# Kernel optimization log

Hardware: AMD Instinct MI355X
Metric: run time of the kernel (lower is better)

The kernel has to match this reference:

```python
import jax, jax.numpy as jnp
import numpy as np

P = 45007
VEC = 4            # default_vec in the triton kernel
BK = 32            # BLOCK_SIZE_K
BN = 32            # BLOCK_SIZE_N
REDN = 2           # reduction factor
IN_FEATURES = 4096
OUT_FEATURES = 4096
RED_IN = ((IN_FEATURES // REDN + BK - 1) // BK) * BK  # 2048


def build_full_idx(random_numbers, K, N, red_in, bk, bn, redn, vec):
    """Vectorized port of SSL.get_idx: flat indices into weight.flatten() for the
    expanded (K, N) weight (i.e. full_weight^T)."""
    R0 = random_numbers[0].astype(jnp.int32)
    R1 = random_numbers[1].astype(jnp.int32)
    R2 = random_numbers[2].astype(jnp.int32)
    R3 = random_numbers[3].astype(jnp.int32)
    ni = K // bk   # number of K blocks
    nj = N // bn   # number of N blocks
    i = jnp.arange(ni, dtype=jnp.int32)
    j = jnp.arange(nj, dtype=jnp.int32)
    it = i // redn                 # [ni]
    itin = i % redn                # [ni]
    h = R3 + R2 * j[None, :] + R1 * (it[:, None] + 1)   # [ni, nj]
    h1 = R0 * (itin + 1)                                 # [ni]
    offset = bk - ((h + h1[:, None]) * vec) % bk         # [ni, nj]
    locs = (offset[:, :, None] + jnp.arange(bk, dtype=jnp.int32)) % bk  # [ni, nj, bk]
    # row index into the compressed weight's reduced-K axis
    row_red = it[:, None, None] * bk + locs              # [ni, nj, bk]
    # reorder so k = i*bk + kk is the leading axis: (ni, bk, nj) -> (K, nj)
    row_red = jnp.transpose(row_red, (0, 2, 1)).reshape(K, nj)
    row_full = jnp.repeat(row_red, bn, axis=1)           # [K, N]
    n_idx = jnp.arange(N, dtype=jnp.int32)[None, :]
    return n_idx * red_in + row_full                     # flat index into weight.flatten()


def setup_inputs() -> dict:
    key = jax.random.key(0)
    k1, k2, k3 = jax.random.split(key, 3)
    x = jax.random.normal(k1, (4, 2048, IN_FEATURES), dtype=jnp.float32)
    # xavier_uniform over (out_features, red_in_features)
    bound_w = float(np.sqrt(6.0 / (OUT_FEATURES + RED_IN)))
    weight = jax.random.uniform(k2, (OUT_FEATURES, RED_IN), dtype=jnp.float32,
                                minval=-bound_w, maxval=bound_w)
    bound_b = 1.0 / float(np.sqrt(IN_FEATURES))
    bias = jax.random.uniform(k3, (OUT_FEATURES,), dtype=jnp.float32,
                              minval=-bound_b, maxval=bound_b)
    # random_numbers = cat([P], 3 ints in [0, P)); fixed representative values
    random_numbers = jnp.array([P, 12345, 6789, 23456], dtype=jnp.int32)
    return {"x": x, "weight": weight, "bias": bias, "random_numbers": random_numbers}


def reference(x, weight, bias, random_numbers):
    K = x.shape[-1]
    N = weight.shape[0]
    full_idx = build_full_idx(random_numbers, K, N, RED_IN, BK, BN, REDN, VEC)  # [K, N]
    w_full = weight.reshape(-1)[full_idx]            # [K, N] = expanded weight^T
    x2 = x.reshape(-1, K)                            # [M, K]
    y = x2 @ w_full + bias[None, :]                  # [M, N]
    return y.reshape(*x.shape[:-1], N)
```

## Files before the change

kernel.cpp:

```cpp
#include <hip/hip_runtime.h>

typedef __bf16 bf16x8 __attribute__((ext_vector_type(8)));
typedef float  f32x4  __attribute__((ext_vector_type(4)));
typedef unsigned short ushort8 __attribute__((ext_vector_type(8)));

#define KDIM  4096
#define NDIM  4096
#define REDIN 2048

static __device__ __forceinline__ unsigned short f2bf(float f) {
    return __builtin_bit_cast(unsigned short, (__bf16)f);
}

typedef __attribute__((address_space(3))) void       lds_void;
typedef const __attribute__((address_space(1))) void gbl_cvoid;

static __device__ __forceinline__ void gload16(const void* g, void* l) {
    __builtin_amdgcn_global_load_lds((gbl_cvoid*)g, (lds_void*)l, 16, 0, 0);
}

__global__ void cvt_x(const float* __restrict__ x, unsigned short* __restrict__ xb,
                      long n8) {
    long idx = (long)blockIdx.x * blockDim.x + threadIdx.x;
    long stride = (long)gridDim.x * blockDim.x;
    for (long i = idx; i < n8; i += stride) {
        const float4 a = ((const float4*)x)[2 * i];
        const float4 b = ((const float4*)x)[2 * i + 1];
        ushort8 s;
        s[0] = f2bf(a.x); s[1] = f2bf(a.y); s[2] = f2bf(a.z); s[3] = f2bf(a.w);
        s[4] = f2bf(b.x); s[5] = f2bf(b.y); s[6] = f2bf(b.z); s[7] = f2bf(b.w);
        ((ushort8*)xb)[i] = s;
    }
}

__global__ void expand_w(const float* __restrict__ w, unsigned short* __restrict__ wx,
                         const int* __restrict__ rn) {
    const int R0 = rn[0], R1 = rn[1], R2 = rn[2], R3 = rn[3];
    const long total = (long)NDIM * (KDIM / 8);
    long idx = (long)blockIdx.x * blockDim.x + threadIdx.x;
    long stride = (long)gridDim.x * blockDim.x;
    for (long t = idx; t < total; t += stride) {
        const int kp = (int)(t & (KDIM / 8 - 1));
        const int n  = (int)(t >> 9);
        const int k0 = kp * 8;
        const int i  = k0 >> 5;
        const int kk0 = k0 & 31;
        const int it = i >> 1;
        const int h  = R3 + R2 * (n >> 5) + R1 * (it + 1) + R0 * ((i & 1) + 1);
        const int off = 32 - ((h << 2) & 31);
        const float* src = w + (long)n * REDIN + it * 32;
        ushort8 s;
#pragma unroll
        for (int q = 0; q < 8; ++q)
            s[q] = f2bf(src[(kk0 + q + off) & 31]);
        ((ushort8*)wx)[t] = s;
    }
}


#define STAGE_T(T)                                                          \
  {                                                                         \
    const int _b  = (T) & 3;                                                \
    const long _ko = (long)(T) * 32;                                        \
    gload16(srcA1 + _ko, ldsA + _b * 8192 + dst1);                          \
    gload16(srcA2 + _ko, ldsA + _b * 8192 + dst2);                          \
    gload16(srcB1 + _ko, ldsB + _b * 8192 + dst1);                          \
    gload16(srcB2 + _ko, ldsB + _b * 8192 + dst2);                          \
  }

#define KBODY(T, CUR, NXT, DOSTAGE, VMSTR)                                  \
  {                                                                         \
    if (DOSTAGE) STAGE_T((T) + 3);                                          \
    asm volatile("s_waitcnt vmcnt(" VMSTR ")" ::: "memory");                \
    __builtin_amdgcn_sched_barrier(0);                                      \
    __builtin_amdgcn_s_barrier();                                           \
    __builtin_amdgcn_sched_barrier(0);                                      \
    const char* _pa = (const char*)ldsA + ((T) & 3) * 16384 + aOff;         \
    const char* _pb = (const char*)ldsB + (((T) + 1) & 3) * 16384 + bOff;   \
    _Pragma("unroll")                                                       \
    for (int _n = 0; _n < 4; ++_n)                                          \
      bf##NXT[_n] = *(const bf16x8*)(_pb + _n * 1024);                      \
    _Pragma("unroll")                                                       \
    for (int _m = 0; _m < 8; ++_m)                                          \
      af[_m] = *(const bf16x8*)(_pa + _m * 1024);                           \
    _Pragma("unroll")                                                       \
    for (int _m = 0; _m < 8; ++_m)                                          \
      _Pragma("unroll")                                                     \
      for (int _n = 0; _n < 4; ++_n)                                        \
        acc[_m][_n] = __builtin_amdgcn_mfma_f32_16x16x32_bf16(              \
            af[_m], bf##CUR[_n], acc[_m][_n], 0, 0, 0);                     \
    asm volatile("s_waitcnt lgkmcnt(0)" ::: "memory");                      \
    __builtin_amdgcn_sched_barrier(0);                                      \
    __builtin_amdgcn_s_barrier();                                           \
  }

__global__ __launch_bounds__(512, 2)
void gemm_bt256(const unsigned short* __restrict__ A,
                const unsigned short* __restrict__ B,
                const float* __restrict__ bias,
                float* __restrict__ out, int M)
{
    __shared__ __align__(16) unsigned short ldsA[4 * 8192];
    __shared__ __align__(16) unsigned short ldsB[4 * 8192];

    const int nwg = gridDim.x;
    const int bid = blockIdx.x;
    int swzb = bid;
    if ((nwg & 7) == 0) {
        const int cpx = nwg >> 3;
        swzb = (bid & 7) * cpx + (bid >> 3);
    }
    const int ntn = NDIM / 256;
    const int n0 = (swzb % ntn) * 256;
    const int m0 = (swzb / ntn) * 256;

    const int tid  = threadIdx.x;
    const int lane = tid & 63;
    const int wid  = tid >> 6;
    const int wr   = wid >> 2;
    const int wc   = wid & 3;
    const int lrow = lane & 15;

    const int sswz = (tid & 3) ^ ((tid >> 3) & 3);
    const int dst1 = tid * 8;
    const int dst2 = tid * 8 + 4096;
    const unsigned short* srcA1 = A + (size_t)(m0 + (tid >> 2)) * KDIM + 8 * sswz;
    const unsigned short* srcA2 = srcA1 + (size_t)128 * KDIM;
    const unsigned short* srcB1 = B + (size_t)(n0 + (tid >> 2)) * KDIM + 8 * sswz;
    const unsigned short* srcB2 = srcB1 + (size_t)128 * KDIM;

    const int rswz = (lane >> 4) ^ ((lane >> 1) & 3);
    const int aOff = (wr * 128 + lrow) * 64 + (rswz << 4);
    const int bOff = (wc * 64 + lrow) * 64 + (rswz << 4);

    f32x4 acc[8][4];
#pragma unroll
    for (int m = 0; m < 8; ++m)
#pragma unroll
        for (int n = 0; n < 4; ++n)
            acc[m][n] = (f32x4)(0.0f);

    bf16x8 af[8], bfA[4], bfB[4];

    STAGE_T(0);
    STAGE_T(1);
    STAGE_T(2);
    asm volatile("s_waitcnt vmcnt(8)" ::: "memory");
    __builtin_amdgcn_sched_barrier(0);
    __builtin_amdgcn_s_barrier();
    __builtin_amdgcn_sched_barrier(0);
    {
        const char* _pb = (const char*)ldsB + bOff;
#pragma unroll
        for (int n = 0; n < 4; ++n)
            bfA[n] = *(const bf16x8*)(_pb + n * 1024);
    }

    for (int tt = 0; tt < 124; tt += 2) {
        KBODY(tt,     A, B, true, "8");
        KBODY(tt + 1, B, A, true, "8");
    }
    KBODY(124, A, B, true,  "8");
    KBODY(125, B, A, false, "4");
    KBODY(126, A, B, false, "0");
    {
        const char* _pa = (const char*)ldsA + 3 * 16384 + aOff;
#pragma unroll
        for (int m = 0; m < 8; ++m)
            af[m] = *(const bf16x8*)(_pa + m * 1024);
#pragma unroll
        for (int m = 0; m < 8; ++m)
#pragma unroll
            for (int n = 0; n < 4; ++n)
                acc[m][n] = __builtin_amdgcn_mfma_f32_16x16x32_bf16(
                    af[m], bfB[n], acc[m][n], 0, 0, 0);
    }

#pragma unroll
    for (int n = 0; n < 4; ++n) {
        const int col = n0 + wc * 64 + n * 16 + lrow;
        const float bv = bias[col];
#pragma unroll
        for (int m = 0; m < 8; ++m) {
            const size_t rbase = (size_t)(m0 + wr * 128 + m * 16 + (lane >> 4) * 4);
#pragma unroll
            for (int e = 0; e < 4; ++e)
                out[(rbase + e) * NDIM + col] = acc[m][n][e] + bv;
        }
    }
}

__global__ __launch_bounds__(256, 2)
void ssl_gemm_fused(const float* __restrict__ x, const float* __restrict__ w,
                    const float* __restrict__ bias, const int* __restrict__ rn,
                    float* __restrict__ out)
{
    __shared__ __align__(16) unsigned short As[128][40];
    __shared__ __align__(16) unsigned short Bs[128][40];

    const int R0 = rn[0], R1 = rn[1], R2 = rn[2], R3 = rn[3];
    const int tid = threadIdx.x;
    const int n0 = blockIdx.x * 128;
    const int m0 = blockIdx.y * 128;
    const int srow = tid >> 3;
    const int scol = (tid & 7) * 4;
    const int lane = tid & 63;
    const int wid  = tid >> 6;
    const int wr   = wid >> 1;
    const int wc   = wid & 1;
    const int lrow = lane & 15;
    const int lk   = (lane >> 4) * 8;

    f32x4 acc[4][4];
#pragma unroll
    for (int m = 0; m < 4; ++m)
#pragma unroll
        for (int n = 0; n < 4; ++n)
            acc[m][n] = (f32x4)(0.0f);

    for (int i = 0; i < KDIM / 32; ++i) {
        const int it   = i >> 1;
        const int k0   = i * 32;
#pragma unroll
        for (int p = 0; p < 4; ++p) {
            const int row = p * 32 + srow;
            const float4 v = *(const float4*)(x + (size_t)(m0 + row) * KDIM + k0 + scol);
            ushort4 s;
            s.x = f2bf(v.x); s.y = f2bf(v.y); s.z = f2bf(v.z); s.w = f2bf(v.w);
            *(ushort4*)&As[row][scol] = s;
        }
        const int hbase = R3 + R1 * (it + 1) + R0 * ((i & 1) + 1);
#pragma unroll
        for (int p = 0; p < 4; ++p) {
            const int nl = p * 32 + srow;
            const int j  = (n0 + nl) >> 5;
            const int off = 32 - (((hbase + R2 * j) << 2) & 31);
            const float4 v = *(const float4*)(w + (size_t)(n0 + nl) * REDIN + it * 32 + scol);
            Bs[nl][(scol + 0 - off) & 31] = f2bf(v.x);
            Bs[nl][(scol + 1 - off) & 31] = f2bf(v.y);
            Bs[nl][(scol + 2 - off) & 31] = f2bf(v.z);
            Bs[nl][(scol + 3 - off) & 31] = f2bf(v.w);
        }
        __syncthreads();

        bf16x8 af[4], bfr[4];
#pragma unroll
        for (int m = 0; m < 4; ++m)
            af[m] = *(const bf16x8*)&As[wr * 64 + m * 16 + lrow][lk];
#pragma unroll
        for (int n = 0; n < 4; ++n)
            bfr[n] = *(const bf16x8*)&Bs[wc * 64 + n * 16 + lrow][lk];
#pragma unroll
        for (int m = 0; m < 4; ++m)
#pragma unroll
            for (int n = 0; n < 4; ++n)
                acc[m][n] = __builtin_amdgcn_mfma_f32_16x16x32_bf16(af[m], bfr[n], acc[m][n], 0, 0, 0);
        __syncthreads();
    }

#pragma unroll
    for (int n = 0; n < 4; ++n) {
        const int col = n0 + wc * 64 + n * 16 + lrow;
        const float bv = bias[col];
#pragma unroll
        for (int m = 0; m < 4; ++m) {
            const int rbase = m0 + wr * 64 + m * 16 + (lane >> 4) * 4;
#pragma unroll
            for (int e = 0; e < 4; ++e)
                out[(size_t)(rbase + e) * NDIM + col] = acc[m][n][e] + bv;
        }
    }
}

extern "C" void kernel_launch(void* const* d_in, const int* in_sizes, int n_in,
                              void* d_out, int out_size, void* d_ws, size_t ws_size,
                              hipStream_t stream) {
    const float* x    = (const float*)d_in[0];
    const float* wgt  = (const float*)d_in[1];
    const float* bias = (const float*)d_in[2];
    const int*   rn   = (const int*)d_in[3];
    float* out = (float*)d_out;

    const int M = in_sizes[0] / KDIM;
    const size_t need = ((size_t)M * KDIM + (size_t)NDIM * KDIM) * sizeof(unsigned short);

    if (ws_size >= need && (M % 256) == 0) {
        unsigned short* xb = (unsigned short*)d_ws;
        unsigned short* wx = xb + (size_t)M * KDIM;

        cvt_x<<<2048, 256, 0, stream>>>(x, xb, (long)M * KDIM / 8);
        expand_w<<<2048, 256, 0, stream>>>(wgt, wx, rn);

        const int nwg = (NDIM / 256) * (M / 256);
        gemm_bt256<<<nwg, 512, 0, stream>>>(xb, wx, bias, out, M);
    } else {
        dim3 grid(NDIM / 128, M / 128);
        ssl_gemm_fused<<<grid, dim3(256), 0, stream>>>(x, wgt, bias, rn, out);
    }
}
```

Baseline: 325.0 us.

## Double-buffer A fragments in registers and raise priority around MFMA blocks

A fragments now use ping-pong register buffers like the B fragments. Each iteration prefetches the next tile's A and B from LDS while the MFMAs consume the current tile, which removes the wait on LDS reads before compute and the explicit lgkmcnt(0) wait. s_setprio is raised around the MFMA block so waves in their compute phase are favoured. The cost is about 32 extra VGPRs per thread at 512 threads with 2 blocks per CU, which risks spills or reduced occupancy.

```diff
diff --git a/kernel.cpp b/kernel.cpp
--- a/kernel.cpp
+++ b/kernel.cpp
@@ -68,29 +68,31 @@
     gload16(srcB2 + _ko, ldsB + _b * 8192 + dst2);                          \
   }
 
-#define KBODY(T, CUR, NXT, DOSTAGE, VMSTR)                                  \
+#define KBODY(T, X, Y, DOSTAGE, VMSTR, DOREAD)                              \
   {                                                                         \
     if (DOSTAGE) STAGE_T((T) + 3);                                          \
     asm volatile("s_waitcnt vmcnt(" VMSTR ")" ::: "memory");                \
     __builtin_amdgcn_sched_barrier(0);                                      \
     __builtin_amdgcn_s_barrier();                                           \
     __builtin_amdgcn_sched_barrier(0);                                      \
-    const char* _pa = (const char*)ldsA + ((T) & 3) * 16384 + aOff;         \
-    const char* _pb = (const char*)ldsB + (((T) + 1) & 3) * 16384 + bOff;   \
-    _Pragma("unroll")                                                       \
-    for (int _n = 0; _n < 4; ++_n)                                          \
-      bf##NXT[_n] = *(const bf16x8*)(_pb + _n * 1024);                      \
-    _Pragma("unroll")                                                       \
-    for (int _m = 0; _m < 8; ++_m)                                          \
-      af[_m] = *(const bf16x8*)(_pa + _m * 1024);                           \
+    if (DOREAD) {                                                           \
+      const char* _pa = (const char*)ldsA + (((T) + 1) & 3) * 16384 + aOff; \
+      const char* _pb = (const char*)ldsB + (((T) + 1) & 3) * 16384 + bOff; \
+      _Pragma("unroll")                                                     \
+      for (int _n = 0; _n < 4; ++_n)                                        \
+        bf##Y[_n] = *(const bf16x8*)(_pb + _n * 1024);                      \
+      _Pragma("unroll")                                                     \
+      for (int _m = 0; _m < 8; ++_m)                                        \
+        af##Y[_m] = *(const bf16x8*)(_pa + _m * 1024);                      \
+    }                                                                       \
+    __builtin_amdgcn_s_setprio(1);                                          \
     _Pragma("unroll")                                                       \
     for (int _m = 0; _m < 8; ++_m)                                          \
       _Pragma("unroll")                                                     \
       for (int _n = 0; _n < 4; ++_n)                                        \
         acc[_m][_n] = __builtin_amdgcn_mfma_f32_16x16x32_bf16(              \
-            af[_m], bf##CUR[_n], acc[_m][_n], 0, 0, 0);                     \
-    asm volatile("s_waitcnt lgkmcnt(0)" ::: "memory");                      \
-    __builtin_amdgcn_sched_barrier(0);                                      \
+            af##X[_m], bf##X[_n], acc[_m][_n], 0, 0, 0);                    \
+    __builtin_amdgcn_s_setprio(0);                                          \
     __builtin_amdgcn_s_barrier();                                           \
   }
 
@@ -140,7 +142,7 @@
         for (int n = 0; n < 4; ++n)
             acc[m][n] = (f32x4)(0.0f);
 
-    bf16x8 af[8], bfA[4], bfB[4];
+    bf16x8 afA[8], afB[8], bfA[4], bfB[4];
 
     STAGE_T(0);
     STAGE_T(1);
@@ -150,30 +152,30 @@
     __builtin_amdgcn_s_barrier();
     __builtin_amdgcn_sched_barrier(0);
     {
+        const char* _pa = (const char*)ldsA + aOff;
         const char* _pb = (const char*)ldsB + bOff;
 #pragma unroll
         for (int n = 0; n < 4; ++n)
             bfA[n] = *(const bf16x8*)(_pb + n * 1024);
+#pragma unroll
+        for (int m = 0; m < 8; ++m)
+            afA[m] = *(const bf16x8*)(_pa + m * 1024);
     }
 
     for (int tt = 0; tt < 124; tt += 2) {
-        KBODY(tt,     A, B, true, "8");
-        KBODY(tt + 1, B, A, true, "8");
-    }
-    KBODY(124, A, B, true,  "8");
-    KBODY(125, B, A, false, "4");
-    KBODY(126, A, B, false, "0");
+        KBODY(tt,     A, B, true, "8", true);
+        KBODY(tt + 1, B, A, true, "8", true);
+    }
+    KBODY(124, A, B, true,  "8", true);
+    KBODY(125, B, A, false, "4", true);
+    KBODY(126, A, B, false, "0", true);
     {
-        const char* _pa = (const char*)ldsA + 3 * 16384 + aOff;
-#pragma unroll
-        for (int m = 0; m < 8; ++m)
-            af[m] = *(const bf16x8*)(_pa + m * 1024);
 #pragma unroll
         for (int m = 0; m < 8; ++m)
 #pragma unroll
             for (int n = 0; n < 4; ++n)
                 acc[m][n] = __builtin_amdgcn_mfma_f32_16x16x32_bf16(
-                    af[m], bfB[n], acc[m][n], 0, 0, 0);
+                    afB[m], bfB[n], acc[m][n], 0, 0, 0);
     }
 
 #pragma unroll
```

After: 340.5 us. 1.05x slower.

## Split K-step MFMA into two half-phases with setprio and drop B-fragment prefetch

Applied to the files above, without the earlier changes.

Restructures the main GEMM loop. B fragments are no longer prefetched one step ahead. Each K-step now loads B plus half of the A fragments, runs 16 MFMAs, then loads the other half of A and runs 16 more, with extra barriers between the halves. MFMA phases are wrapped in s_setprio(1) so the compute wave gets priority while other waves issue LDS/global loads. The vmcnt waits are retuned to keep three stages in flight. This lowers fragment register use but adds barriers and serializes each LDS read against the MFMAs that consume it.

```diff
diff --git a/kernel.cpp b/kernel.cpp
--- a/kernel.cpp
+++ b/kernel.cpp
@@ -68,7 +68,7 @@
     gload16(srcB2 + _ko, ldsB + _b * 8192 + dst2);                          \
   }
 
-#define KBODY(T, CUR, NXT, DOSTAGE, VMSTR)                                  \
+#define KBODY(T, DOSTAGE, VMSTR)                                            \
   {                                                                         \
     if (DOSTAGE) STAGE_T((T) + 3);                                          \
     asm volatile("s_waitcnt vmcnt(" VMSTR ")" ::: "memory");                \
@@ -76,22 +76,41 @@
     __builtin_amdgcn_s_barrier();                                           \
     __builtin_amdgcn_sched_barrier(0);                                      \
     const char* _pa = (const char*)ldsA + ((T) & 3) * 16384 + aOff;         \
-    const char* _pb = (const char*)ldsB + (((T) + 1) & 3) * 16384 + bOff;   \
+    const char* _pb = (const char*)ldsB + ((T) & 3) * 16384 + bOff;         \
+    bf16x8 _bf[4], _af[4];                                                  \
     _Pragma("unroll")                                                       \
     for (int _n = 0; _n < 4; ++_n)                                          \
-      bf##NXT[_n] = *(const bf16x8*)(_pb + _n * 1024);                      \
-    _Pragma("unroll")                                                       \
-    for (int _m = 0; _m < 8; ++_m)                                          \
-      af[_m] = *(const bf16x8*)(_pa + _m * 1024);                           \
-    _Pragma("unroll")                                                       \
-    for (int _m = 0; _m < 8; ++_m)                                          \
+      _bf[_n] = *(const bf16x8*)(_pb + _n * 1024);                          \
+    _Pragma("unroll")                                                       \
+    for (int _m = 0; _m < 4; ++_m)                                          \
+      _af[_m] = *(const bf16x8*)(_pa + _m * 1024);                          \
+    asm volatile("s_waitcnt lgkmcnt(0)" ::: "memory");                      \
+    __builtin_amdgcn_sched_barrier(0);                                      \
+    __builtin_amdgcn_s_setprio(1);                                          \
+    _Pragma("unroll")                                                       \
+    for (int _m = 0; _m < 4; ++_m)                                          \
       _Pragma("unroll")                                                     \
       for (int _n = 0; _n < 4; ++_n)                                        \
         acc[_m][_n] = __builtin_amdgcn_mfma_f32_16x16x32_bf16(              \
-            af[_m], bf##CUR[_n], acc[_m][_n], 0, 0, 0);                     \
+            _af[_m], _bf[_n], acc[_m][_n], 0, 0, 0);                        \
+    __builtin_amdgcn_s_setprio(0);                                          \
+    __builtin_amdgcn_s_barrier();                                           \
+    __builtin_amdgcn_sched_barrier(0);                                      \
+    _Pragma("unroll")                                                       \
+    for (int _m = 0; _m < 4; ++_m)                                          \
+      _af[_m] = *(const bf16x8*)(_pa + 4096 + _m * 1024);                   \
     asm volatile("s_waitcnt lgkmcnt(0)" ::: "memory");                      \
     __builtin_amdgcn_sched_barrier(0);                                      \
+    __builtin_amdgcn_s_setprio(1);                                          \
+    _Pragma("unroll")                                                       \
+    for (int _m = 0; _m < 4; ++_m)                                          \
+      _Pragma("unroll")                                                     \
+      for (int _n = 0; _n < 4; ++_n)                                        \
+        acc[4 + _m][_n] = __builtin_amdgcn_mfma_f32_16x16x32_bf16(          \
+            _af[_m], _bf[_n], acc[4 + _m][_n], 0, 0, 0);                    \
+    __builtin_amdgcn_s_setprio(0);                                          \
     __builtin_amdgcn_s_barrier();                                           \
+    __builtin_amdgcn_sched_barrier(0);                                      \
   }
 
 __global__ __launch_bounds__(512, 2)
@@ -140,41 +159,16 @@
         for (int n = 0; n < 4; ++n)
             acc[m][n] = (f32x4)(0.0f);
 
-    bf16x8 af[8], bfA[4], bfB[4];
-
     STAGE_T(0);
     STAGE_T(1);
     STAGE_T(2);
-    asm volatile("s_waitcnt vmcnt(8)" ::: "memory");
-    __builtin_amdgcn_sched_barrier(0);
-    __builtin_amdgcn_s_barrier();
-    __builtin_amdgcn_sched_barrier(0);
-    {
-        const char* _pb = (const char*)ldsB + bOff;
-#pragma unroll
-        for (int n = 0; n < 4; ++n)
-            bfA[n] = *(const bf16x8*)(_pb + n * 1024);
-    }
-
-    for (int tt = 0; tt < 124; tt += 2) {
-        KBODY(tt,     A, B, true, "8");
-        KBODY(tt + 1, B, A, true, "8");
-    }
-    KBODY(124, A, B, true,  "8");
-    KBODY(125, B, A, false, "4");
-    KBODY(126, A, B, false, "0");
-    {
-        const char* _pa = (const char*)ldsA + 3 * 16384 + aOff;
-#pragma unroll
-        for (int m = 0; m < 8; ++m)
-            af[m] = *(const bf16x8*)(_pa + m * 1024);
-#pragma unroll
-        for (int m = 0; m < 8; ++m)
-#pragma unroll
-            for (int n = 0; n < 4; ++n)
-                acc[m][n] = __builtin_amdgcn_mfma_f32_16x16x32_bf16(
-                    af[m], bfB[n], acc[m][n], 0, 0, 0);
-    }
+
+    for (int t = 0; t < 125; ++t) {
+        KBODY(t, true, "12");
+    }
+    KBODY(125, false, "8");
+    KBODY(126, false, "4");
+    KBODY(127, false, "0");
 
 #pragma unroll
     for (int n = 0; n < 4; ++n) {
```

New measurement: 381.4 us. 17.3% more time.
